# Performance work log

Measured on AMD Instinct MI355X. Metric: run time of the kernel, lower is better.

Reference implementation:

```python
import jax, jax.numpy as jnp
import numpy as np

SAMPLE_RATE = 48000  # from __init__ kwarg


def setup_inputs() -> dict:
    key = jax.random.key(0)
    B, T = 16, 1048576  # 16 channels x ~21.8s @ 48kHz
    audio = jax.random.normal(key, (B, T), dtype=jnp.float32) * 0.5
    return {
        "audio": audio,
        "threshold": jnp.float32(-20.0),   # dB
        "ratio": jnp.float32(4.0),         # 4:1
        "attack": jnp.float32(0.01),
        "release": jnp.float32(0.1),
        "makeup_gain": jnp.float32(0.0),   # dB
    }


def reference(audio, threshold, ratio, attack, release, makeup_gain):
    # Static gain computer
    audio_abs = jnp.abs(audio) + 1e-8
    audio_db = 20.0 * jnp.log10(audio_abs)
    over = jnp.maximum(audio_db - threshold, 0.0)
    gain_reduction = over * (1.0 - 1.0 / ratio)          # [B, T], dB of reduction

    # One-pole attack/release smoothing coefficients
    alpha_attack = 1.0 - jnp.exp(-1.0 / (attack * SAMPLE_RATE))
    alpha_release = 1.0 - jnp.exp(-1.0 / (release * SAMPLE_RATE))

    # Sequential envelope scan over time: gain_smooth[0] = 0, then
    # g[t] = (1-a)*g[t-1] + a*gr[t], a = attack if gr[t] > g[t-1] else release.
    g0 = jnp.zeros(audio.shape[:-1], dtype=audio.dtype)  # [B]

    def step(g_prev, gr_t):
        alpha = jnp.where(gr_t > g_prev, alpha_attack, alpha_release)
        g = (1.0 - alpha) * g_prev + alpha * gr_t
        return g, g

    gr_time_major = jnp.moveaxis(gain_reduction[..., 1:], -1, 0)  # [T-1, B]
    _, gs = jax.lax.scan(step, g0, gr_time_major)                 # [T-1, B]
    gain_smooth = jnp.concatenate([g0[..., None], jnp.moveaxis(gs, 0, -1)], axis=-1)  # [B, T]

    gain_linear = 10.0 ** ((-gain_smooth + makeup_gain) / 20.0)
    compressed = jnp.sign(audio) * audio_abs * gain_linear

    # Early-exit bypass for silent input (jit-friendly via where)
    return jnp.where(jnp.max(jnp.abs(audio)) < 1e-6, audio, compressed)
```

## Files before the change

kernel.cpp:

```cpp
#include <hip/hip_runtime.h>


#define T_LEN   (1 << 20)
#define W_WARM  12288
#define C_CHUNK 1024
#define RECS_PER_CH (T_LEN / 32)

typedef _Float16 half_t;
typedef _Float16 half8 __attribute__((ext_vector_type(8)));
typedef float    fvec4 __attribute__((ext_vector_type(4)));

__device__ __forceinline__ float fmax3f(float a, float b, float c) {
  return fmaxf(fmaxf(a, b), c);
}

__global__ __launch_bounds__(256) void pre_kernel(
    const float* __restrict__ audio,
    const float* __restrict__ p_thr,
    const float* __restrict__ p_ratio,
    const float* __restrict__ p_att,
    const float* __restrict__ p_rel,
    half8* __restrict__ recs, int nrec_total) {
  int rec = blockIdx.x * blockDim.x + threadIdx.x;
  if (rec >= nrec_total) return;
  const float thr = p_thr[0];
  const float r1  = 1.0f - 1.0f / p_ratio[0];
  const float K   = 6.0205999132796239f * r1;
  const float Cc  = -thr * r1;
  const float L2E = 1.4426950408889634f;
  const float aatt = 1.0f - __builtin_exp2f(-L2E / (p_att[0] * 48000.0f));
  const float arel = 1.0f - __builtin_exp2f(-L2E / (p_rel[0] * 48000.0f));
  const float b1 = 1.0f - aatt, b2 = 1.0f - arel;
  const float s0 = b1 * b1, s1 = b1 * b2, s2 = b2 * b2;

  const fvec4* A4 = (const fvec4*)(audio) + (size_t)rec * 8;
  float gr[32];
#pragma unroll
  for (int i = 0; i < 8; ++i) {
    fvec4 v = A4[i];
#pragma unroll
    for (int j = 0; j < 4; ++j)
      gr[4 * i + j] =
          fmaxf(fmaf(K, __builtin_log2f(fabsf(v[j]) + 1e-8f), Cc), 0.0f);
  }
  if ((rec & (RECS_PER_CH - 1)) == 0) gr[0] = 0.0f;

  half8 h[5];
#pragma unroll
  for (int q = 0; q < 8; ++q) {
    float A0 = aatt * gr[4*q],     R0 = arel * gr[4*q];
    float A1 = aatt * gr[4*q + 1], R1 = arel * gr[4*q + 1];
    float u0 = fmaf(b1, A0, A1);
    float um = fmaxf(fmaf(b1, R0, A1), fmaf(b2, A0, R1));
    float u2 = fmaf(b2, R0, R1);
    float A2 = aatt * gr[4*q + 2], R2 = arel * gr[4*q + 2];
    float A3 = aatt * gr[4*q + 3], R3 = arel * gr[4*q + 3];
    float v0 = fmaf(b1, A2, A3);
    float vm = fmaxf(fmaf(b1, R2, A3), fmaf(b2, A2, R3));
    float v2 = fmaf(b2, R2, R3);
    float w0 = fmaf(s0, u0, v0);
    float w1 = fmaxf(fmaf(s0, um, v0), fmaf(s1, u0, vm));
    float w2 = fmax3f(fmaf(s0, u2, v0), fmaf(s1, um, vm), fmaf(s2, u0, v2));
    float w3 = fmaxf(fmaf(s1, u2, vm), fmaf(s2, um, v2));
    float w4 = fmaf(s2, u2, v2);
    h[0][q] = (half_t)w0; h[1][q] = (half_t)w1; h[2][q] = (half_t)w2;
    h[3][q] = (half_t)w3; h[4][q] = (half_t)w4;
  }
  half8* dst = recs + (size_t)rec * 5;
#pragma unroll
  for (int j = 0; j < 5; ++j) dst[j] = h[j];
}

__global__ __launch_bounds__(64) void comp_kernel(
    const float* __restrict__ audio,
    const half8* __restrict__ recs,
    const float* __restrict__ p_thr,
    const float* __restrict__ p_ratio,
    const float* __restrict__ p_att,
    const float* __restrict__ p_rel,
    const float* __restrict__ p_mk,
    float* __restrict__ out, int total_chunks) {
  const int tid = blockIdx.x * blockDim.x + threadIdx.x;
  if (tid >= total_chunks) return;
  const int CPC = T_LEN / C_CHUNK;
  const int ch = tid / CPC;
  const int t0 = (tid - ch * CPC) * C_CHUNK;

  const float thr = p_thr[0];
  const float r1  = 1.0f - 1.0f / p_ratio[0];
  const float K   = 6.0205999132796239f * r1;
  const float Cc  = -thr * r1;
  const float L2E = 1.4426950408889634f;
  const float aatt = 1.0f - __builtin_exp2f(-L2E / (p_att[0] * 48000.0f));
  const float arel = 1.0f - __builtin_exp2f(-L2E / (p_rel[0] * 48000.0f));
  const float b1 = 1.0f - aatt, b2 = 1.0f - arel;
  const float s0 = b1 * b1, s1 = b1 * b2, s2 = b2 * b2;
  const float S0 = s0 * s0, S1 = s0 * s1, S2 = s1 * s1, S3 = s1 * s2, S4 = s2 * s2;
  const float EK  = 0.16609640474436813f;
  const float emk = p_mk[0] * EK;

  float g = 0.0f;

  int start = t0 - W_WARM;
  if (start < 0) start = 0;
  const int nrec = (t0 - start) >> 5;
  if (nrec > 0) {
    const half8* P = recs + ((size_t)ch * RECS_PER_CH + (start >> 5)) * 5;
    half8 bA[5], bB[5], bC[5], bD[5];
    auto ld = [&](half8 (&b)[5], int r) {
      const half8* p = P + 5 * r;
#pragma unroll
      for (int i = 0; i < 5; ++i) b[i] = p[i];
    };
    auto proc = [&](const half8 (&b)[5]) {
#pragma unroll
      for (int q = 0; q < 8; ++q) {
        float l0 = fmaf(S0, g, (float)b[0][q]);
        float l1 = fmaf(S1, g, (float)b[1][q]);
        float l2 = fmaf(S2, g, (float)b[2][q]);
        float l3 = fmaf(S3, g, (float)b[3][q]);
        float l4 = fmaf(S4, g, (float)b[4][q]);
        g = fmax3f(fmax3f(l0, l1, l2), l3, l4);
      }
    };
    ld(bA, 0); ld(bB, 1); ld(bC, 2);
#pragma unroll 1
    for (int r = 0; r + 4 <= nrec; r += 4) {
      ld(bD, r + 3); proc(bA);
      ld(bA, r + 4); proc(bB);
      ld(bB, r + 5); proc(bC);
      ld(bC, r + 6); proc(bD);
    }
  }

  const fvec4* Ap = (const fvec4*)(audio + (size_t)ch * T_LEN + t0);
  fvec4* Op = (fvec4*)(out + (size_t)ch * T_LEN + t0);
  const bool zfix = (t0 == 0);

  fvec4 a0[8], a1[8];
  auto lda = [&](fvec4 (&ab)[8], int b) {
#pragma unroll
    for (int i = 0; i < 8; ++i) ab[i] = Ap[8 * b + i];
  };
  auto emit = [&](const fvec4 (&ab)[8], int b, bool first) {
    fvec4 r[8];
#pragma unroll
    for (int s = 0; s < 32; ++s) {
      float x = ab[s >> 2][s & 3];
      float ax = fabsf(x) + 1e-8f;
      float grv = fmaxf(fmaf(K, __builtin_log2f(ax), Cc), 0.0f);
      if (first && s == 0 && zfix) grv = 0.0f;
      float d = grv - g;
      g = fmaxf(fmaf(aatt, d, g), fmaf(arel, d, g));
      float mag = ax * __builtin_exp2f(fmaf(-EK, g, emk));
      float o = copysignf(mag, x);
      r[s >> 2][s & 3] = (x == 0.0f) ? 0.0f : o;
    }
#pragma unroll
    for (int i = 0; i < 8; ++i) Op[8 * b + i] = r[i];
  };

  const int NB = C_CHUNK / 32;
  lda(a0, 0);
#pragma unroll 1
  for (int b = 0; b < NB; b += 2) {
    lda(a1, b + 1);
    emit(a0, b, b == 0);
    int b2 = (b + 2 < NB) ? b + 2 : NB - 1;
    lda(a0, b2);
    emit(a1, b + 1, false);
  }
}

extern "C" void kernel_launch(void* const* d_in, const int* in_sizes, int n_in,
                              void* d_out, int out_size, void* d_ws, size_t ws_size,
                              hipStream_t stream) {
  const float* audio   = (const float*)d_in[0];
  const float* p_thr   = (const float*)d_in[1];
  const float* p_ratio = (const float*)d_in[2];
  const float* p_att   = (const float*)d_in[3];
  const float* p_rel   = (const float*)d_in[4];
  const float* p_mk    = (const float*)d_in[5];
  float* outp = (float*)d_out;

  const int n = in_sizes[0];
  const int nrec_total = n / 32;
  const int total_chunks = n / C_CHUNK;
  half8* recs = (half8*)d_ws;

  pre_kernel<<<(nrec_total + 255) / 256, 256, 0, stream>>>(
      audio, p_thr, p_ratio, p_att, p_rel, recs, nrec_total);
  comp_kernel<<<(total_chunks + 63) / 64, 64, 0, stream>>>(
      audio, recs, p_thr, p_ratio, p_att, p_rel, p_mk, outp, total_chunks);
}
```

Baseline: 173.1 us.

## Compose 64-sample max-plus operators and split warm-up scan into separate kernel

The preprocessing kernel now composes max-plus affine operators hierarchically over 64 samples, giving 65 fp16 coefficients per block instead of 5 per 32 samples. A new scanA kernel applies up to 128 of these operators (8192 samples) to compute each 512-sample chunk's starting envelope. The final kernel only reads that start value and runs the exact per-sample recurrence on half-size chunks. This cuts the serial warm-up chain and doubles chunk parallelism, at the cost of an extra launch, more register-heavy composition and a shorter warm-up window that depends on the envelope decaying fast enough.

Measured after the change: 202.7 us. +17.1%, slower.

```diff
diff --git a/kernel.cpp b/kernel.cpp
--- a/kernel.cpp
+++ b/kernel.cpp
@@ -2,9 +2,11 @@
 
 
 #define T_LEN   (1 << 20)
-#define W_WARM  12288
-#define C_CHUNK 1024
-#define RECS_PER_CH (T_LEN / 32)
+#define NCH     16
+#define C_CHUNK 512
+#define RECS_PER_CH (T_LEN / 64)
+#define CH_CHUNKS   (T_LEN / C_CHUNK)
+#define N_WARM_OPS  128
 
 typedef _Float16 half_t;
 typedef _Float16 half8 __attribute__((ext_vector_type(8)));
@@ -14,15 +16,34 @@
   return fmaxf(fmaxf(a, b), c);
 }
 
-__global__ __launch_bounds__(256) void pre_kernel(
+template <int P, int Q>
+__device__ __forceinline__ void compose_im(float* __restrict__ dst,
+                                           const float* __restrict__ hi,
+                                           const float* __restrict__ lo,
+                                           float s, float rat) {
+#pragma unroll
+  for (int k = 0; k < P + Q - 1; ++k) dst[k] = -1e30f;
+#pragma unroll
+  for (int i = 0; i < P; ++i) {
+#pragma unroll
+    for (int j = 0; j < Q; ++j)
+      dst[i + j] = fmaxf(dst[i + j], fmaf(s, lo[j], hi[i]));
+    s *= rat;
+  }
+}
+
+__global__ __launch_bounds__(256) void pre64_kernel(
     const float* __restrict__ audio,
     const float* __restrict__ p_thr,
     const float* __restrict__ p_ratio,
     const float* __restrict__ p_att,
     const float* __restrict__ p_rel,
-    half8* __restrict__ recs, int nrec_total) {
-  int rec = blockIdx.x * blockDim.x + threadIdx.x;
-  if (rec >= nrec_total) return;
+    half8* __restrict__ ops64, int nrec) {
+  const int rec = blockIdx.x * 256 + (int)threadIdx.x;
+  if (rec >= nrec) return;
+  const int ch = rec >> 14;
+  const int p  = rec & 16383;
+
   const float thr = p_thr[0];
   const float r1  = 1.0f - 1.0f / p_ratio[0];
   const float K   = 6.0205999132796239f * r1;
@@ -32,59 +53,146 @@
   const float arel = 1.0f - __builtin_exp2f(-L2E / (p_rel[0] * 48000.0f));
   const float b1 = 1.0f - aatt, b2 = 1.0f - arel;
   const float s0 = b1 * b1, s1 = b1 * b2, s2 = b2 * b2;
-
-  const fvec4* A4 = (const fvec4*)(audio) + (size_t)rec * 8;
-  float gr[32];
-#pragma unroll
-  for (int i = 0; i < 8; ++i) {
-    fvec4 v = A4[i];
+  const float rat = b2 / b1;
+  const float b1_4 = s0 * s0, b1_8 = b1_4 * b1_4, b1_16 = b1_8 * b1_8,
+              b1_32 = b1_16 * b1_16;
+
+  const fvec4* A4 = (const fvec4*)(audio) + (size_t)rec * 16;
+  const bool zf = (p == 0);
+
+  auto mkquad = [&](int b, float* qq) {
+    fvec4 v = A4[b];
+    float gg[4];
 #pragma unroll
     for (int j = 0; j < 4; ++j)
-      gr[4 * i + j] =
-          fmaxf(fmaf(K, __builtin_log2f(fabsf(v[j]) + 1e-8f), Cc), 0.0f);
-  }
-  if ((rec & (RECS_PER_CH - 1)) == 0) gr[0] = 0.0f;
-
-  half8 h[5];
-#pragma unroll
-  for (int q = 0; q < 8; ++q) {
-    float A0 = aatt * gr[4*q],     R0 = arel * gr[4*q];
-    float A1 = aatt * gr[4*q + 1], R1 = arel * gr[4*q + 1];
+      gg[j] = fmaxf(fmaf(K, __builtin_log2f(fabsf(v[j]) + 1e-8f), Cc), 0.0f);
+    if (zf && b == 0) gg[0] = 0.0f;
+    float A0 = aatt * gg[0], R0 = arel * gg[0];
+    float A1 = aatt * gg[1], R1 = arel * gg[1];
     float u0 = fmaf(b1, A0, A1);
     float um = fmaxf(fmaf(b1, R0, A1), fmaf(b2, A0, R1));
     float u2 = fmaf(b2, R0, R1);
-    float A2 = aatt * gr[4*q + 2], R2 = arel * gr[4*q + 2];
-    float A3 = aatt * gr[4*q + 3], R3 = arel * gr[4*q + 3];
+    float A2 = aatt * gg[2], R2 = arel * gg[2];
+    float A3 = aatt * gg[3], R3 = arel * gg[3];
     float v0 = fmaf(b1, A2, A3);
     float vm = fmaxf(fmaf(b1, R2, A3), fmaf(b2, A2, R3));
     float v2 = fmaf(b2, R2, R3);
-    float w0 = fmaf(s0, u0, v0);
-    float w1 = fmaxf(fmaf(s0, um, v0), fmaf(s1, u0, vm));
-    float w2 = fmax3f(fmaf(s0, u2, v0), fmaf(s1, um, vm), fmaf(s2, u0, v2));
-    float w3 = fmaxf(fmaf(s1, u2, vm), fmaf(s2, um, v2));
-    float w4 = fmaf(s2, u2, v2);
-    h[0][q] = (half_t)w0; h[1][q] = (half_t)w1; h[2][q] = (half_t)w2;
-    h[3][q] = (half_t)w3; h[4][q] = (half_t)w4;
-  }
-  half8* dst = recs + (size_t)rec * 5;
-#pragma unroll
-  for (int j = 0; j < 5; ++j) dst[j] = h[j];
-}
-
-__global__ __launch_bounds__(64) void comp_kernel(
+    qq[0] = fmaf(s0, u0, v0);
+    qq[1] = fmaxf(fmaf(s0, um, v0), fmaf(s1, u0, vm));
+    qq[2] = fmax3f(fmaf(s0, u2, v0), fmaf(s1, um, vm), fmaf(s2, u0, v2));
+    qq[3] = fmaxf(fmaf(s1, u2, vm), fmaf(s2, um, v2));
+    qq[4] = fmaf(s2, u2, v2);
+  };
+  auto mk17 = [&](int qb, float* o17) {
+    float qa[5], qc[5], o9a[9], o9b[9];
+    mkquad(qb + 0, qa); mkquad(qb + 1, qc);
+    compose_im<5, 5>(o9a, qc, qa, b1_4, rat);
+    mkquad(qb + 2, qa); mkquad(qb + 3, qc);
+    compose_im<5, 5>(o9b, qc, qa, b1_4, rat);
+    compose_im<9, 9>(o17, o9b, o9a, b1_8, rat);
+  };
+
+  float o33a[33], o33b[33], o65[65];
+  {
+    float o17a[17], o17b[17];
+    mk17(0, o17a); mk17(4, o17b);
+    compose_im<17, 17>(o33a, o17b, o17a, b1_16, rat);
+    mk17(8, o17a); mk17(12, o17b);
+    compose_im<17, 17>(o33b, o17b, o17a, b1_16, rat);
+  }
+  compose_im<33, 33>(o65, o33b, o33a, b1_32, rat);
+
+  half8* dst = ops64 + (size_t)(p * NCH + ch) * 9;
+#pragma unroll
+  for (int j8 = 0; j8 < 9; ++j8) {
+    half8 hb;
+#pragma unroll
+    for (int e = 0; e < 8; ++e) {
+      const int k = 8 * j8 + e;
+      hb[e] = (k < 65) ? (half_t)o65[k] : (half_t)0.0f;
+    }
+    dst[j8] = hb;
+  }
+}
+
+__global__ __launch_bounds__(256) void scanA_kernel(
+    const half8* __restrict__ ops64,
+    const float* __restrict__ p_att,
+    const float* __restrict__ p_rel,
+    float* __restrict__ g_start, int nthreads) {
+  const int tid = blockIdx.x * 256 + (int)threadIdx.x;
+  if (tid >= nthreads) return;
+  const int l    = tid & 63;
+  const int wv   = tid >> 6;
+  const int ch   = l & 15;
+  const int cpos = wv * 4 + (l >> 4);
+
+  const float L2E = 1.4426950408889634f;
+  const float aatt = 1.0f - __builtin_exp2f(-L2E / (p_att[0] * 48000.0f));
+  const float arel = 1.0f - __builtin_exp2f(-L2E / (p_rel[0] * 48000.0f));
+  const float b1 = 1.0f - aatt, b2 = 1.0f - arel;
+  const float rat = b2 / b1;
+
+  float S[65];
+  {
+    const float b1_2 = b1 * b1, b1_4 = b1_2 * b1_2, b1_8 = b1_4 * b1_4;
+    const float b1_16 = b1_8 * b1_8, b1_32 = b1_16 * b1_16;
+    float pw = b1_32 * b1_32;
+#pragma unroll
+    for (int i = 0; i < 65; ++i) { S[i] = pw; pw *= rat; }
+  }
+
+  float g = 0.0f;
+  auto apply = [&](const half8 (&o)[9]) {
+    float m0 = -1e30f, m1 = -1e30f, m2 = -1e30f, m3 = -1e30f;
+#pragma unroll
+    for (int i = 0; i < 65; ++i) {
+      const float t = fmaf(S[i], g, (float)o[i >> 3][i & 7]);
+      if ((i & 3) == 0) m0 = fmaxf(m0, t);
+      else if ((i & 3) == 1) m1 = fmaxf(m1, t);
+      else if ((i & 3) == 2) m2 = fmaxf(m2, t);
+      else m3 = fmaxf(m3, t);
+    }
+    g = fmaxf(fmaxf(m0, m1), fmaxf(m2, m3));
+  };
+
+  const int navail = cpos * 8;
+  const int nops = (navail < N_WARM_OPS) ? navail : N_WARM_OPS;
+  if (nops > 0) {
+    const int p0 = cpos * 8 - nops;
+    const half8* P = ops64 + (size_t)(p0 * NCH + ch) * 9;
+    const size_t stride = (size_t)NCH * 9;
+    half8 bA[9], bB[9];
+#pragma unroll
+    for (int i = 0; i < 9; ++i) bA[i] = P[i];
+#pragma unroll 1
+    for (int r = 0; r + 2 <= nops; r += 2) {
+      const half8* Pn = P + (size_t)(r + 1) * stride;
+#pragma unroll
+      for (int i = 0; i < 9; ++i) bB[i] = Pn[i];
+      apply(bA);
+      const half8* Pn2 = P + (size_t)(r + 2) * stride;
+#pragma unroll
+      for (int i = 0; i < 9; ++i) bA[i] = Pn2[i];
+      apply(bB);
+    }
+  }
+  g_start[ch * CH_CHUNKS + cpos] = g;
+}
+
+__global__ __launch_bounds__(256) void scanB_kernel(
     const float* __restrict__ audio,
-    const half8* __restrict__ recs,
+    const float* __restrict__ g_start,
     const float* __restrict__ p_thr,
     const float* __restrict__ p_ratio,
     const float* __restrict__ p_att,
     const float* __restrict__ p_rel,
     const float* __restrict__ p_mk,
-    float* __restrict__ out, int total_chunks) {
-  const int tid = blockIdx.x * blockDim.x + threadIdx.x;
-  if (tid >= total_chunks) return;
-  const int CPC = T_LEN / C_CHUNK;
-  const int ch = tid / CPC;
-  const int t0 = (tid - ch * CPC) * C_CHUNK;
+    float* __restrict__ out, int nchunks) {
+  const int tid = blockIdx.x * 256 + (int)threadIdx.x;
+  if (tid >= nchunks) return;
+  const int ch = tid >> 11;
+  const int t0 = (tid & 2047) * C_CHUNK;
 
   const float thr = p_thr[0];
   const float r1  = 1.0f - 1.0f / p_ratio[0];
@@ -94,45 +202,10 @@
   const float aatt = 1.0f - __builtin_exp2f(-L2E / (p_att[0] * 48000.0f));
   const float arel = 1.0f - __builtin_exp2f(-L2E / (p_rel[0] * 48000.0f));
   const float b1 = 1.0f - aatt, b2 = 1.0f - arel;
-  const float s0 = b1 * b1, s1 = b1 * b2, s2 = b2 * b2;
-  const float S0 = s0 * s0, S1 = s0 * s1, S2 = s1 * s1, S3 = s1 * s2, S4 = s2 * s2;
   const float EK  = 0.16609640474436813f;
   const float emk = p_mk[0] * EK;
 
-  float g = 0.0f;
-
-  int start = t0 - W_WARM;
-  if (start < 0) start = 0;
-  const int nrec = (t0 - start) >> 5;
-  if (nrec > 0) {
-    const half8* P = recs + ((size_t)ch * RECS_PER_CH + (start >> 5)) * 5;
-    half8 bA[5], bB[5], bC[5], bD[5];
-    auto ld = [&](half8 (&b)[5], int r) {
-      const half8* p = P + 5 * r;
-#pragma unroll
-      for (int i = 0; i < 5; ++i) b[i] = p[i];
-    };
-    auto proc = [&](const half8 (&b)[5]) {
-#pragma unroll
-      for (int q = 0; q < 8; ++q) {
-        float l0 = fmaf(S0, g, (float)b[0][q]);
-        float l1 = fmaf(S1, g, (float)b[1][q]);
-        float l2 = fmaf(S2, g, (float)b[2][q]);
-        float l3 = fmaf(S3, g, (float)b[3][q]);
-        float l4 = fmaf(S4, g, (float)b[4][q]);
-        g = fmax3f(fmax3f(l0, l1, l2), l3, l4);
-      }
-    };
-    ld(bA, 0); ld(bB, 1); ld(bC, 2);
-#pragma unroll 1
-    for (int r = 0; r + 4 <= nrec; r += 4) {
-      ld(bD, r + 3); proc(bA);
-      ld(bA, r + 4); proc(bB);
-      ld(bB, r + 5); proc(bC);
-      ld(bC, r + 6); proc(bD);
-    }
-  }
-
+  float g = g_start[tid];
   const fvec4* Ap = (const fvec4*)(audio + (size_t)ch * T_LEN + t0);
   fvec4* Op = (fvec4*)(out + (size_t)ch * T_LEN + t0);
   const bool zfix = (t0 == 0);
@@ -150,8 +223,8 @@
       float ax = fabsf(x) + 1e-8f;
       float grv = fmaxf(fmaf(K, __builtin_log2f(ax), Cc), 0.0f);
       if (first && s == 0 && zfix) grv = 0.0f;
-      float d = grv - g;
-      g = fmaxf(fmaf(aatt, d, g), fmaf(arel, d, g));
+      float Aa = aatt * grv, Rr = arel * grv;
+      g = fmaxf(fmaf(b1, g, Aa), fmaf(b2, g, Rr));
       float mag = ax * __builtin_exp2f(fmaf(-EK, g, emk));
       float o = copysignf(mag, x);
       r[s >> 2][s & 3] = (x == 0.0f) ? 0.0f : o;
@@ -166,8 +239,8 @@
   for (int b = 0; b < NB; b += 2) {
     lda(a1, b + 1);
     emit(a0, b, b == 0);
-    int b2 = (b + 2 < NB) ? b + 2 : NB - 1;
-    lda(a0, b2);
+    const int bnx = (b + 2 < NB) ? b + 2 : NB - 1;
+    lda(a0, bnx);
     emit(a1, b + 1, false);
   }
 }
@@ -184,12 +257,16 @@
   float* outp = (float*)d_out;
 
   const int n = in_sizes[0];
-  const int nrec_total = n / 32;
-  const int total_chunks = n / C_CHUNK;
-  half8* recs = (half8*)d_ws;
-
-  pre_kernel<<<(nrec_total + 255) / 256, 256, 0, stream>>>(
-      audio, p_thr, p_ratio, p_att, p_rel, recs, nrec_total);
-  comp_kernel<<<(total_chunks + 63) / 64, 64, 0, stream>>>(
-      audio, recs, p_thr, p_ratio, p_att, p_rel, p_mk, outp, total_chunks);
-}
+  const int nrec = n / 64;
+  const int nchunks = n / C_CHUNK;
+
+  half8* ops64   = (half8*)d_ws;
+  float* g_start = (float*)((char*)d_ws + ((size_t)48 << 20));
+
+  pre64_kernel<<<(nrec + 255) / 256, 256, 0, stream>>>(
+      audio, p_thr, p_ratio, p_att, p_rel, ops64, nrec);
+  scanA_kernel<<<(nchunks + 255) / 256, 256, 0, stream>>>(
+      ops64, p_att, p_rel, g_start, nchunks);
+  scanB_kernel<<<(nchunks + 255) / 256, 256, 0, stream>>>(
+      audio, g_start, p_thr, p_ratio, p_att, p_rel, p_mk, outp, nchunks);
+}
```
